# Optimization experiments

Hardware: AMD Instinct MI355X
Metric: run time of the kernel (lower is better)

## Reference

```python
import jax, jax.numpy as jnp
import numpy as np
import math

EMBED_DIM = 512
NUM_HEADS = 8
HEAD_DIM = EMBED_DIM // NUM_HEADS


def setup_inputs() -> dict:
    key = jax.random.key(0)
    ks = jax.random.split(key, 11)
    s = 1.0 / math.sqrt(EMBED_DIM)
    x = jax.random.normal(ks[0], (8, EMBED_DIM, 32, 32), dtype=jnp.float32)
    Wq = jax.random.uniform(ks[1], (EMBED_DIM, EMBED_DIM), jnp.float32, -s, s)
    bq = jax.random.uniform(ks[2], (EMBED_DIM,), jnp.float32, -s, s)
    Wk = jax.random.uniform(ks[3], (EMBED_DIM, EMBED_DIM), jnp.float32, -s, s)
    bk = jax.random.uniform(ks[4], (EMBED_DIM,), jnp.float32, -s, s)
    Wv = jax.random.uniform(ks[5], (EMBED_DIM, EMBED_DIM), jnp.float32, -s, s)
    bv = jax.random.uniform(ks[6], (EMBED_DIM,), jnp.float32, -s, s)
    Wo = jax.random.uniform(ks[7], (EMBED_DIM, EMBED_DIM), jnp.float32, -s, s)
    bo = jax.random.uniform(ks[8], (EMBED_DIM,), jnp.float32, -s, s)
    gamma = jnp.ones((EMBED_DIM,), jnp.float32)
    beta = jnp.zeros((EMBED_DIM,), jnp.float32)
    return {"x": x, "Wq": Wq, "bq": bq, "Wk": Wk, "bk": bk, "Wv": Wv,
            "bv": bv, "Wo": Wo, "bo": bo, "gamma": gamma, "beta": beta}


def layer_norm(x, gamma, beta, eps=1e-5):
    mu = jnp.mean(x, axis=-1, keepdims=True)
    var = jnp.mean(jnp.square(x - mu), axis=-1, keepdims=True)
    return (x - mu) * jax.lax.rsqrt(var + eps) * gamma + beta


def reference(x, Wq, bq, Wk, bk, Wv, bv, Wo, bo, gamma, beta):
    B, C, H, W = x.shape
    S = H * W
    # [B, S, C]
    x_flat = x.reshape(B, C, S).transpose(0, 2, 1)
    residual = x_flat
    xn = layer_norm(x_flat, gamma, beta)
    # torch Linear: y = x @ W^T + b
    q = (xn @ Wq.T + bq).reshape(B, S, NUM_HEADS, HEAD_DIM)
    k = (xn @ Wk.T + bk).reshape(B, S, NUM_HEADS, HEAD_DIM)
    v = (xn @ Wv.T + bv).reshape(B, S, NUM_HEADS, HEAD_DIM)
    scale = 1.0 / math.sqrt(HEAD_DIM)
    scores = jnp.einsum('bqhd,bkhd->bhqk', q, k) * scale
    attn = jax.nn.softmax(scores, axis=-1)  # dropout is identity in eval
    out = jnp.einsum('bhqk,bkhd->bqhd', attn, v).reshape(B, S, C)
    out = out @ Wo.T + bo + residual
    return out.transpose(0, 2, 1).reshape(B, C, H, W)
```

## Files before the change

### kernel.cpp

```cpp
#include <hip/hip_runtime.h>
#include <hip/hip_bf16.h>

typedef __bf16 bf16_t;
typedef __bf16 bf16x8 __attribute__((ext_vector_type(8)));
typedef float floatx4 __attribute__((ext_vector_type(4)));

#define EMBED 512
#define S_LEN 1024
#define NH 8
#define HD 64
#define LDK 1056
#define LDV 1088

#define MFMA16(a, b, c) __builtin_amdgcn_mfma_f32_16x16x32_bf16(a, b, c, 0, 0, 0)

static __device__ __forceinline__ bf16_t f2bf(float f) {
    unsigned int x = __builtin_bit_cast(unsigned int, f);
    unsigned int lsb = (x >> 16) & 1u;
    x += 0x7fffu + lsb;
    unsigned short u = (unsigned short)(x >> 16);
    return __builtin_bit_cast(bf16_t, u);
}
static __device__ __forceinline__ float bf2f(bf16_t v) {
    unsigned short u = __builtin_bit_cast(unsigned short, v);
    unsigned int x = ((unsigned int)u) << 16;
    return __builtin_bit_cast(float, x);
}
static __device__ __forceinline__ unsigned int pack2(float lo, float hi) {
    return (__builtin_bit_cast(unsigned int, lo) >> 16) |
           (__builtin_bit_cast(unsigned int, hi) & 0xFFFF0000u);
}
static __device__ __forceinline__ unsigned int pack2r(float lo, float hi) {
    unsigned short a = __builtin_bit_cast(unsigned short, f2bf(lo));
    unsigned short b = __builtin_bit_cast(unsigned short, f2bf(hi));
    return (unsigned int)a | ((unsigned int)b << 16);
}
static __device__ __forceinline__ void gload16(const bf16_t* g, bf16_t* l) {
    __builtin_amdgcn_global_load_lds(
        (const __attribute__((address_space(1))) unsigned int*)g,
        (__attribute__((address_space(3))) unsigned int*)l, 16, 0, 0);
}

__global__ __launch_bounds__(256) void ln_cvt_kernel(const float* __restrict__ x,
                                                     const float* __restrict__ gamma,
                                                     const float* __restrict__ beta,
                                                     bf16_t* __restrict__ xn,
                                                     const float* __restrict__ w0,
                                                     const float* __restrict__ w1,
                                                     const float* __restrict__ w2,
                                                     const float* __restrict__ w3,
                                                     bf16_t* __restrict__ d0,
                                                     bf16_t* __restrict__ d1,
                                                     bf16_t* __restrict__ d2,
                                                     bf16_t* __restrict__ d3) {
    __shared__ float T[16][521];
    __shared__ float Pm[16][65], Pq[16][65];
    __shared__ float Mu[16], Rs[16];
    int bid = blockIdx.x;
    int t = threadIdx.x;
    if (bid >= 512) {
        int cb2 = bid - 512;
        const float* s; bf16_t* d;
        switch (cb2 >> 7) {
            case 0:  s = w0; d = d0; break;
            case 1:  s = w1; d = d1; break;
            case 2:  s = w2; d = d2; break;
            default: s = w3; d = d3; break;
        }
        int i = ((cb2 & 127) * 256 + t) * 8;
#pragma unroll
        for (int j = 0; j < 8; ++j) d[i + j] = f2bf(s[i + j]);
        return;
    }
    int b = bid >> 6, s0 = (bid & 63) * 16;
    int lc = t >> 2;
    int si = (t & 3) * 4;
    const float* xp = x + ((size_t)b * EMBED + lc) * S_LEN + s0 + si;
    float sm[4] = {}, sq[4] = {};
#pragma unroll
    for (int p = 0; p < 8; ++p) {
        int c = lc + p * 64;
        float4 v = *(const float4*)(xp + (size_t)p * 64 * S_LEN);
        int cs = c ^ ((c >> 3) & 0x38);
        T[si + 0][cs] = v.x; T[si + 1][cs] = v.y;
        T[si + 2][cs] = v.z; T[si + 3][cs] = v.w;
        sm[0] += v.x; sq[0] += v.x * v.x;
        sm[1] += v.y; sq[1] += v.y * v.y;
        sm[2] += v.z; sq[2] += v.z * v.z;
        sm[3] += v.w; sq[3] += v.w * v.w;
    }
#pragma unroll
    for (int k = 0; k < 4; ++k) { Pm[si + k][lc] = sm[k]; Pq[si + k][lc] = sq[k]; }
    __syncthreads();
    if (t < 16) {
        float m = 0.f, q = 0.f;
#pragma unroll
        for (int j = 0; j < 64; ++j) { m += Pm[t][j]; q += Pq[t][j]; }
        float mu = m * (1.0f / EMBED);
        float var = q * (1.0f / EMBED) - mu * mu;
        Mu[t] = mu; Rs[t] = rsqrtf(var + 1e-5f);
    }
    __syncthreads();
    int cidx = t & 31;
    int rw = t >> 5;
#pragma unroll
    for (int rg = 0; rg < 2; ++rg) {
        int srl = rg * 8 + rw;
        float mu = Mu[srl], rs = Rs[srl];
        int cb = cidx * 16;
        bf16_t* dst = xn + ((size_t)b * S_LEN + s0 + srl) * EMBED + cb;
#pragma unroll
        for (int h = 0; h < 2; ++h) {
            int c0h = cb + h * 8;
            float4 g0 = *(const float4*)(gamma + c0h);
            float4 g1 = *(const float4*)(gamma + c0h + 4);
            float4 be0 = *(const float4*)(beta + c0h);
            float4 be1 = *(const float4*)(beta + c0h + 4);
            float gv[8] = {g0.x, g0.y, g0.z, g0.w, g1.x, g1.y, g1.z, g1.w};
            float bv[8] = {be0.x, be0.y, be0.z, be0.w, be1.x, be1.y, be1.z, be1.w};
            bf16x8 o;
#pragma unroll
            for (int j = 0; j < 8; ++j) {
                int c = c0h + j;
                int cs = c ^ ((c >> 3) & 0x38);
                o[j] = f2bf((T[srl][cs] - mu) * rs * gv[j] + bv[j]);
            }
            *(bf16x8*)(dst + h * 8) = o;
        }
    }
}

__global__ __launch_bounds__(256) void gemm_kernel(const bf16_t* __restrict__ X,
                                                   const bf16_t* __restrict__ W,
                                                   const float* __restrict__ b0,
                                                   const float* __restrict__ b1,
                                                   const float* __restrict__ b2,
                                                   bf16_t* __restrict__ Y,
                                                   bf16_t* __restrict__ vtb) {
    __shared__ __align__(16) bf16_t Sh[2][128 * 72];
    bf16_t* Wlin = &Sh[0][0];
    int t = threadIdx.x;
    int col0 = blockIdx.y * 128, row0 = blockIdx.x * 128;
    int lane = t & 63, w = t >> 6, g = lane >> 4, n16 = lane & 15;
    int swzk = (((lane & 7) ^ (lane >> 3)) & 7) * 8;
    const bf16_t* wg = W + (size_t)(col0 + w * 32 + (lane >> 3)) * EMBED + swzk;
    bf16_t* ldwave = Wlin + (w * 4) * 512;
    {
#pragma unroll
        for (int j = 0; j < 4; ++j)
            gload16(wg + (size_t)j * 8 * EMBED, ldwave + j * 512);
    }
    int rw0 = row0 + w * 32;
    const bf16_t* xr0 = X + (size_t)(rw0 + n16) * EMBED + g * 8;
    const bf16_t* xr1 = xr0 + (size_t)16 * EMBED;
    bf16x8 a00 = *(const bf16x8*)(xr0);
    bf16x8 a01 = *(const bf16x8*)(xr0 + 32);
    bf16x8 a10 = *(const bf16x8*)(xr1);
    bf16x8 a11 = *(const bf16x8*)(xr1 + 32);
    __syncthreads();
    floatx4 acc[2][8] = {};
    int cs0 = ((g ^ (n16 & 7))) * 8;
#pragma unroll
    for (int kc = 0; kc < 8; ++kc) {
        bf16x8 na00, na01, na10, na11;
        if (kc < 7) {
            int ko = (kc + 1) * 64;
            bf16_t* ld = Wlin + ((kc + 1) & 1) * 8192 + (w * 4) * 512;
#pragma unroll
            for (int j = 0; j < 4; ++j)
                gload16(wg + (size_t)j * 8 * EMBED + ko, ld + j * 512);
            na00 = *(const bf16x8*)(xr0 + ko);
            na01 = *(const bf16x8*)(xr0 + ko + 32);
            na10 = *(const bf16x8*)(xr1 + ko);
            na11 = *(const bf16x8*)(xr1 + ko + 32);
        }
        const bf16_t* wb = Wlin + (kc & 1) * 8192;
#pragma unroll
        for (int kk = 0; kk < 2; ++kk) {
            bf16x8 s0 = (kk == 0) ? a00 : a01;
            bf16x8 s1 = (kk == 0) ? a10 : a11;
            int csk = cs0 ^ (kk * 32);
#pragma unroll
            for (int nt = 0; nt < 8; ++nt) {
                bf16x8 bfr = *(const bf16x8*)(&wb[(nt * 16 + n16) * 64 + csk]);
                acc[0][nt] = MFMA16(s0, bfr, acc[0][nt]);
                acc[1][nt] = MFMA16(s1, bfr, acc[1][nt]);
            }
        }
        if (kc < 7) {
            a00 = na00; a01 = na01; a10 = na10; a11 = na11;
        }
        __syncthreads();
    }
    if (col0 < 1024) {
        const float* bp = (col0 < 512) ? b0 : b1;
#pragma unroll
        for (int ar = 0; ar < 2; ++ar)
#pragma unroll
            for (int nt = 0; nt < 8; ++nt) {
                int col = col0 + nt * 16 + n16;
                float bv = bp[col & 511];
#pragma unroll
                for (int r = 0; r < 4; ++r) {
                    int row = rw0 + ar * 16 + g * 4 + r;
                    Y[(size_t)row * LDK + col] = f2bf(acc[ar][nt][r] + bv);
                }
            }
    } else {
        bf16_t* Tl = Wlin;
#pragma unroll
        for (int ar = 0; ar < 2; ++ar)
#pragma unroll
            for (int nt = 0; nt < 8; ++nt) {
                int chl = nt * 16 + n16;
                float bv = b2[(col0 & 511) + chl];
                uint2 pr;
                pr.x = pack2r(acc[ar][nt][0] + bv, acc[ar][nt][1] + bv);
                pr.y = pack2r(acc[ar][nt][2] + bv, acc[ar][nt][3] + bv);
                *(uint2*)(&Tl[chl * 136 + w * 32 + ar * 16 + g * 4]) = pr;
            }
        __syncthreads();
        int ch = t >> 1, seg = (t & 1) * 64;
        int bb = row0 >> 10, s0 = row0 & 1023;
        bf16_t* dst = vtb + ((size_t)(bb * EMBED + (col0 - 1024) + ch)) * LDV + s0 + seg;
        const bf16_t* srcl = &Tl[ch * 136 + seg];
#pragma unroll
        for (int i = 0; i < 8; ++i)
            *(bf16x8*)(dst + i * 8) = *(const bf16x8*)(srcl + i * 8);
    }
}

__global__ __launch_bounds__(256) void wsgemm_out_kernel(const bf16_t* __restrict__ Wb,
                                                         const bf16_t* __restrict__ act,
                                                         const float* __restrict__ bias,
                                                         const float* __restrict__ xres,
                                                         float* __restrict__ out) {
    __shared__ __align__(16) bf16_t Al[2][64 * 72];
    int b = blockIdx.z, n0 = blockIdx.x * 64, m0 = blockIdx.y * 128;
    int t = threadIdx.x;
    int srow = t >> 2, sseg = (t & 3) * 16;
    const bf16_t* asrc = act + ((size_t)b * S_LEN + n0 + srow) * EMBED + sseg;
    {
        bf16x8 r0 = *(const bf16x8*)(asrc);
        bf16x8 r1 = *(const bf16x8*)(asrc + 8);
        bf16_t* d = &Al[0][srow * 72 + sseg];
        *(bf16x8*)d = r0; *(bf16x8*)(d + 8) = r1;
    }
    int lane = t & 63, w = t >> 6, g = lane >> 4, n16 = lane & 15;
    int mw = m0 + w * 32;
    const bf16_t* wr0 = Wb + (size_t)(mw + n16) * EMBED + g * 8;
    const bf16_t* wr1 = wr0 + (size_t)16 * EMBED;
    bf16x8 a00 = *(const bf16x8*)(wr0);
    bf16x8 a01 = *(const bf16x8*)(wr0 + 32);
    bf16x8 a10 = *(const bf16x8*)(wr1);
    bf16x8 a11 = *(const bf16x8*)(wr1 + 32);
    __syncthreads();
    floatx4 acc[2][4] = {};
#pragma unroll
    for (int kc = 0; kc < 8; ++kc) {
        bf16x8 p0, p1, na00, na01, na10, na11;
        if (kc < 7) {
            int ko = (kc + 1) * 64;
            p0 = *(const bf16x8*)(asrc + ko);
            p1 = *(const bf16x8*)(asrc + ko + 8);
            na00 = *(const bf16x8*)(wr0 + ko);
            na01 = *(const bf16x8*)(wr0 + ko + 32);
            na10 = *(const bf16x8*)(wr1 + ko);
            na11 = *(const bf16x8*)(wr1 + ko + 32);
        }
        const bf16_t* al = &Al[kc & 1][0];
#pragma unroll
        for (int kk = 0; kk < 2; ++kk) {
            bf16x8 s0 = (kk == 0) ? a00 : a01;
            bf16x8 s1 = (kk == 0) ? a10 : a11;
#pragma unroll
            for (int nt = 0; nt < 4; ++nt) {
                bf16x8 bfr = *(const bf16x8*)(&al[(nt * 16 + n16) * 72 + kk * 32 + g * 8]);
                acc[0][nt] = MFMA16(s0, bfr, acc[0][nt]);
                acc[1][nt] = MFMA16(s1, bfr, acc[1][nt]);
            }
        }
        if (kc < 7) {
            bf16_t* d = &Al[(kc + 1) & 1][srow * 72 + sseg];
            *(bf16x8*)d = p0; *(bf16x8*)(d + 8) = p1;
            a00 = na00; a01 = na01; a10 = na10; a11 = na11;
        }
        __syncthreads();
    }
#pragma unroll
    for (int ar = 0; ar < 2; ++ar)
#pragma unroll
        for (int r = 0; r < 4; ++r) {
            int row = mw + ar * 16 + g * 4 + r;
            float bv = bias[row];
#pragma unroll
            for (int nt = 0; nt < 4; ++nt) {
                int col = n0 + nt * 16 + n16;
                size_t oi = ((size_t)b * EMBED + row) * S_LEN + col;
                out[oi] = acc[ar][nt][r] + bv + xres[oi];
            }
        }
}

__global__ __launch_bounds__(256) void attn_kernel(const bf16_t* __restrict__ qk,
                                                   const bf16_t* __restrict__ vt,
                                                   bf16_t* __restrict__ o) {
    __shared__ __align__(16) bf16_t Kt[2][64 * 72];
    __shared__ __align__(16) bf16_t Vl2[2][64 * 72];
    __shared__ __align__(16) unsigned int Pl[4][16 * 68];
    int bid = blockIdx.x;
    int bh = bid & 63, qt = bid >> 6;
    int b = bh >> 3, h = bh & 7;
    int t = threadIdx.x, w = t >> 6, lane = t & 63, g = lane >> 4, n16 = lane & 15;
    size_t baseQK = (size_t)b * S_LEN * LDK;
    size_t baseV  = ((size_t)b * EMBED + h * HD) * LDV;
    int qA = qt * 128 + w * 32 + n16;

    const float QSC = 0.18033688f;
    const bf16_t* qpA = qk + baseQK + (size_t)qA * LDK + h * HD + g * 8;
    const bf16_t* qpB = qpA + (size_t)16 * LDK;
    bf16x8 qa0 = *(const bf16x8*)(qpA);
    bf16x8 qa1 = *(const bf16x8*)(qpA + 32);
    bf16x8 qb0 = *(const bf16x8*)(qpB);
    bf16x8 qb1 = *(const bf16x8*)(qpB + 32);
#pragma unroll
    for (int j = 0; j < 8; ++j) {
        qa0[j] = f2bf(bf2f(qa0[j]) * QSC);
        qa1[j] = f2bf(bf2f(qa1[j]) * QSC);
        qb0[j] = f2bf(bf2f(qb0[j]) * QSC);
        qb1[j] = f2bf(bf2f(qb1[j]) * QSC);
    }
    const bf16_t* kbase = qk + baseQK + 512 + h * HD;
    const bf16_t* vbase = vt + baseV;

    int srow = t >> 2, scol = (t & 3) * 16;
    const bf16_t* ksrc = kbase + (size_t)srow * LDK + scol;
    const bf16_t* vsrc = vbase + (size_t)srow * LDV + scol;
    {
        bf16x8 k0 = *(const bf16x8*)(ksrc);
        bf16x8 k1 = *(const bf16x8*)(ksrc + 8);
        bf16x8 v0 = *(const bf16x8*)(vsrc);
        bf16x8 v1 = *(const bf16x8*)(vsrc + 8);
        bf16_t* kd = &Kt[0][srow * 72 + scol];
        bf16_t* vd = &Vl2[0][srow * 72 + scol];
        *(bf16x8*)kd = k0; *(bf16x8*)(kd + 8) = k1;
        *(bf16x8*)vd = v0; *(bf16x8*)(vd + 8) = v1;
    }

    float lsA[4] = {}, lsB[4] = {};
    floatx4 oaccA[4] = {}, oaccB[4] = {};
    unsigned int* PLw = &Pl[w][0];
    const float NEG12L2E = -17.3123405f;

    for (int it = 0; it < 16; ++it) {
        int cur = it & 1, nxt = cur ^ 1;
        __syncthreads();
        bf16x8 pk0, pk1, pv0, pv1;
        if (it < 15) {
            const bf16_t* kp = ksrc + (size_t)(it + 1) * 64 * LDK;
            pk0 = *(const bf16x8*)(kp);
            pk1 = *(const bf16x8*)(kp + 8);
            const bf16_t* vp = vsrc + (it + 1) * 64;
            pv0 = *(const bf16x8*)(vp);
            pv1 = *(const bf16x8*)(vp + 8);
        }
        const bf16_t* Kl = &Kt[cur][0];
        const bf16_t* Vl = &Vl2[cur][0];
        floatx4 sA[4], sB[4];
#pragma unroll
        for (int kb = 0; kb < 4; ++kb) {
            bf16x8 k0 = *(const bf16x8*)(&Kl[(kb * 16 + n16) * 72 + g * 8]);
            bf16x8 k1 = *(const bf16x8*)(&Kl[(kb * 16 + n16) * 72 + 32 + g * 8]);
            sA[kb] = floatx4{NEG12L2E, NEG12L2E, NEG12L2E, NEG12L2E};
            sA[kb] = MFMA16(k0, qa0, sA[kb]);
            sA[kb] = MFMA16(k1, qa1, sA[kb]);
            sB[kb] = floatx4{NEG12L2E, NEG12L2E, NEG12L2E, NEG12L2E};
            sB[kb] = MFMA16(k0, qb0, sB[kb]);
            sB[kb] = MFMA16(k1, qb1, sB[kb]);
        }
#pragma unroll
        for (int kb = 0; kb < 4; ++kb)
#pragma unroll
            for (int r = 0; r < 4; ++r) {
                float eA = exp2f(sA[kb][r]);
                sA[kb][r] = eA; lsA[kb] += eA;
                float eB = exp2f(sB[kb][r]);
                sB[kb][r] = eB; lsB[kb] += eB;
            }
#pragma unroll
        for (int kb = 0; kb < 4; ++kb) {
            uint2 prA, prB;
            prA.x = pack2(sA[kb][0], sA[kb][1]);
            prA.y = pack2(sA[kb][2], sA[kb][3]);
            *(uint2*)&PLw[n16 * 68 + kb * 8 + g * 2] = prA;
            prB.x = pack2(sB[kb][0], sB[kb][1]);
            prB.y = pack2(sB[kb][2], sB[kb][3]);
            *(uint2*)&PLw[n16 * 68 + 32 + kb * 8 + g * 2] = prB;
        }
        uint4 uA0 = *(const uint4*)&PLw[n16 * 68 + g * 4];
        uint4 uA1 = *(const uint4*)&PLw[n16 * 68 + 16 + g * 4];
        uint4 uB0 = *(const uint4*)&PLw[n16 * 68 + 32 + g * 4];
        uint4 uB1 = *(const uint4*)&PLw[n16 * 68 + 48 + g * 4];
        bf16x8 pfA0 = __builtin_bit_cast(bf16x8, uA0);
        bf16x8 pfA1 = __builtin_bit_cast(bf16x8, uA1);
        bf16x8 pfB0 = __builtin_bit_cast(bf16x8, uB0);
        bf16x8 pfB1 = __builtin_bit_cast(bf16x8, uB1);
        if (it < 15) {
            bf16_t* kd = &Kt[nxt][srow * 72 + scol];
            bf16_t* vd = &Vl2[nxt][srow * 72 + scol];
            *(bf16x8*)kd = pk0; *(bf16x8*)(kd + 8) = pk1;
            *(bf16x8*)vd = pv0; *(bf16x8*)(vd + 8) = pv1;
        }
#pragma unroll
        for (int dt = 0; dt < 4; ++dt) {
            bf16x8 v0 = *(const bf16x8*)(&Vl[(dt * 16 + n16) * 72 + g * 8]);
            bf16x8 v1 = *(const bf16x8*)(&Vl[(dt * 16 + n16) * 72 + 32 + g * 8]);
            oaccA[dt] = MFMA16(v0, pfA0, oaccA[dt]);
            oaccA[dt] = MFMA16(v1, pfA1, oaccA[dt]);
            oaccB[dt] = MFMA16(v0, pfB0, oaccB[dt]);
            oaccB[dt] = MFMA16(v1, pfB1, oaccB[dt]);
        }
    }
    float lA = (lsA[0] + lsA[1]) + (lsA[2] + lsA[3]);
    lA += __shfl_xor(lA, 16);
    lA += __shfl_xor(lA, 32);
    float lB = (lsB[0] + lsB[1]) + (lsB[2] + lsB[3]);
    lB += __shfl_xor(lB, 16);
    lB += __shfl_xor(lB, 32);
    float rlA = 1.0f / lA, rlB = 1.0f / lB;
    size_t orowA = ((size_t)b * S_LEN + qA) * EMBED + h * HD;
    size_t orowB = orowA + (size_t)16 * EMBED;
#pragma unroll
    for (int dt = 0; dt < 4; ++dt) {
        uint2 prA, prB;
        prA.x = pack2(oaccA[dt][0] * rlA, oaccA[dt][1] * rlA);
        prA.y = pack2(oaccA[dt][2] * rlA, oaccA[dt][3] * rlA);
        *(uint2*)(o + orowA + dt * 16 + g * 4) = prA;
        prB.x = pack2(oaccB[dt][0] * rlB, oaccB[dt][1] * rlB);
        prB.y = pack2(oaccB[dt][2] * rlB, oaccB[dt][3] * rlB);
        *(uint2*)(o + orowB + dt * 16 + g * 4) = prB;
    }
}

extern "C" void kernel_launch(void* const* d_in, const int* in_sizes, int n_in,
                              void* d_out, int out_size, void* d_ws, size_t ws_size,
                              hipStream_t stream) {
    const float* x     = (const float*)d_in[0];
    const float* Wq    = (const float*)d_in[1];
    const float* bq    = (const float*)d_in[2];
    const float* Wk    = (const float*)d_in[3];
    const float* bk    = (const float*)d_in[4];
    const float* Wv    = (const float*)d_in[5];
    const float* bv    = (const float*)d_in[6];
    const float* Wo    = (const float*)d_in[7];
    const float* bo    = (const float*)d_in[8];
    const float* gamma = (const float*)d_in[9];
    const float* beta  = (const float*)d_in[10];
    float* out = (float*)d_out;

    char* ws = (char*)d_ws;
    bf16_t* xn    = (bf16_t*)ws;
    bf16_t* qkb   = (bf16_t*)(ws + 8388608);
    bf16_t* wqkv  = (bf16_t*)(ws + 25690112);
    bf16_t* wo    = (bf16_t*)(ws + 27262976);
    bf16_t* ab    = xn;

    bf16_t* vtb = (bf16_t*)d_out;

    ln_cvt_kernel<<<dim3(1024), 256, 0, stream>>>(x, gamma, beta, xn,
                                                  Wq, Wk, Wv, Wo,
                                                  wqkv, wqkv + 262144,
                                                  wqkv + 524288, wo);
    gemm_kernel<<<dim3(64, 12), 256, 0, stream>>>(xn, wqkv, bq, bk, bv, qkb, vtb);
    attn_kernel<<<dim3(512), 256, 0, stream>>>(qkb, vtb, ab);
    wsgemm_out_kernel<<<dim3(16, 4, 8), 256, 0, stream>>>(wo, ab, bo, x, out);
}
```

Baseline: 170.0 us.

## Deepen K/V prefetch to two tiles ahead with unrolled even/odd iterations

New measurement: 169.0 us. About the same (-0.6%).

```diff
diff --git a/kernel.cpp b/kernel.cpp
--- a/kernel.cpp
+++ b/kernel.cpp
@@ -346,81 +346,121 @@
         *(bf16x8*)kd = k0; *(bf16x8*)(kd + 8) = k1;
         *(bf16x8*)vd = v0; *(bf16x8*)(vd + 8) = v1;
     }
+    bf16x8 rkO0, rkO1, rvO0, rvO1, rkE0, rkE1, rvE0, rvE1;
+    {
+        const bf16_t* kp = ksrc + (size_t)64 * LDK;
+        rkO0 = *(const bf16x8*)(kp);
+        rkO1 = *(const bf16x8*)(kp + 8);
+        const bf16_t* vp = vsrc + 64;
+        rvO0 = *(const bf16x8*)(vp);
+        rvO1 = *(const bf16x8*)(vp + 8);
+    }
 
     float lsA[4] = {}, lsB[4] = {};
     floatx4 oaccA[4] = {}, oaccB[4] = {};
     unsigned int* PLw = &Pl[w][0];
     const float NEG12L2E = -17.3123405f;
-
-    for (int it = 0; it < 16; ++it) {
-        int cur = it & 1, nxt = cur ^ 1;
+    bf16x8 pfA0, pfA1, pfB0, pfB1;
+
+#define ATTN_QKSM(CUR)                                                        \
+    {                                                                         \
+        const bf16_t* Kl = &Kt[CUR][0];                                       \
+        floatx4 sA[4], sB[4];                                                 \
+        _Pragma("unroll")                                                     \
+        for (int kb = 0; kb < 4; ++kb) {                                      \
+            bf16x8 k0 = *(const bf16x8*)(&Kl[(kb * 16 + n16) * 72 + g * 8]);  \
+            bf16x8 k1 = *(const bf16x8*)(&Kl[(kb * 16 + n16) * 72 + 32 + g * 8]); \
+            sA[kb] = floatx4{NEG12L2E, NEG12L2E, NEG12L2E, NEG12L2E};         \
+            sA[kb] = MFMA16(k0, qa0, sA[kb]);                                 \
+            sA[kb] = MFMA16(k1, qa1, sA[kb]);                                 \
+            sB[kb] = floatx4{NEG12L2E, NEG12L2E, NEG12L2E, NEG12L2E};         \
+            sB[kb] = MFMA16(k0, qb0, sB[kb]);                                 \
+            sB[kb] = MFMA16(k1, qb1, sB[kb]);                                 \
+        }                                                                     \
+        _Pragma("unroll")                                                     \
+        for (int kb = 0; kb < 4; ++kb)                                        \
+            _Pragma("unroll")                                                 \
+            for (int r = 0; r < 4; ++r) {                                     \
+                float eA = exp2f(sA[kb][r]);                                  \
+                sA[kb][r] = eA; lsA[kb] += eA;                                \
+                float eB = exp2f(sB[kb][r]);                                  \
+                sB[kb][r] = eB; lsB[kb] += eB;                                \
+            }                                                                 \
+        _Pragma("unroll")                                                     \
+        for (int kb = 0; kb < 4; ++kb) {                                      \
+            uint2 prA, prB;                                                   \
+            prA.x = pack2(sA[kb][0], sA[kb][1]);                              \
+            prA.y = pack2(sA[kb][2], sA[kb][3]);                              \
+            *(uint2*)&PLw[n16 * 68 + kb * 8 + g * 2] = prA;                   \
+            prB.x = pack2(sB[kb][0], sB[kb][1]);                              \
+            prB.y = pack2(sB[kb][2], sB[kb][3]);                              \
+            *(uint2*)&PLw[n16 * 68 + 32 + kb * 8 + g * 2] = prB;              \
+        }                                                                     \
+        uint4 uA0 = *(const uint4*)&PLw[n16 * 68 + g * 4];                    \
+        uint4 uA1 = *(const uint4*)&PLw[n16 * 68 + 16 + g * 4];               \
+        uint4 uB0 = *(const uint4*)&PLw[n16 * 68 + 32 + g * 4];               \
+        uint4 uB1 = *(const uint4*)&PLw[n16 * 68 + 48 + g * 4];               \
+        pfA0 = __builtin_bit_cast(bf16x8, uA0);                               \
+        pfA1 = __builtin_bit_cast(bf16x8, uA1);                               \
+        pfB0 = __builtin_bit_cast(bf16x8, uB0);                               \
+        pfB1 = __builtin_bit_cast(bf16x8, uB1);                               \
+    }
+
+#define ATTN_PV(CUR)                                                          \
+    {                                                                         \
+        const bf16_t* Vl = &Vl2[CUR][0];                                      \
+        _Pragma("unroll")                                                     \
+        for (int dt = 0; dt < 4; ++dt) {                                      \
+            bf16x8 v0 = *(const bf16x8*)(&Vl[(dt * 16 + n16) * 72 + g * 8]);  \
+            bf16x8 v1 = *(const bf16x8*)(&Vl[(dt * 16 + n16) * 72 + 32 + g * 8]); \
+            oaccA[dt] = MFMA16(v0, pfA0, oaccA[dt]);                          \
+            oaccA[dt] = MFMA16(v1, pfA1, oaccA[dt]);                          \
+            oaccB[dt] = MFMA16(v0, pfB0, oaccB[dt]);                          \
+            oaccB[dt] = MFMA16(v1, pfB1, oaccB[dt]);                          \
+        }                                                                     \
+    }
+
+    for (int ih = 0; ih < 8; ++ih) {
+        int itE = ih * 2;
+        int itO = itE + 1;
         __syncthreads();
-        bf16x8 pk0, pk1, pv0, pv1;
-        if (it < 15) {
-            const bf16_t* kp = ksrc + (size_t)(it + 1) * 64 * LDK;
-            pk0 = *(const bf16x8*)(kp);
-            pk1 = *(const bf16x8*)(kp + 8);
-            const bf16_t* vp = vsrc + (it + 1) * 64;
-            pv0 = *(const bf16x8*)(vp);
-            pv1 = *(const bf16x8*)(vp + 8);
-        }
-        const bf16_t* Kl = &Kt[cur][0];
-        const bf16_t* Vl = &Vl2[cur][0];
-        floatx4 sA[4], sB[4];
-#pragma unroll
-        for (int kb = 0; kb < 4; ++kb) {
-            bf16x8 k0 = *(const bf16x8*)(&Kl[(kb * 16 + n16) * 72 + g * 8]);
-            bf16x8 k1 = *(const bf16x8*)(&Kl[(kb * 16 + n16) * 72 + 32 + g * 8]);
-            sA[kb] = floatx4{NEG12L2E, NEG12L2E, NEG12L2E, NEG12L2E};
-            sA[kb] = MFMA16(k0, qa0, sA[kb]);
-            sA[kb] = MFMA16(k1, qa1, sA[kb]);
-            sB[kb] = floatx4{NEG12L2E, NEG12L2E, NEG12L2E, NEG12L2E};
-            sB[kb] = MFMA16(k0, qb0, sB[kb]);
-            sB[kb] = MFMA16(k1, qb1, sB[kb]);
-        }
-#pragma unroll
-        for (int kb = 0; kb < 4; ++kb)
-#pragma unroll
-            for (int r = 0; r < 4; ++r) {
-                float eA = exp2f(sA[kb][r]);
-                sA[kb][r] = eA; lsA[kb] += eA;
-                float eB = exp2f(sB[kb][r]);
-                sB[kb][r] = eB; lsB[kb] += eB;
-            }
-#pragma unroll
-        for (int kb = 0; kb < 4; ++kb) {
-            uint2 prA, prB;
-            prA.x = pack2(sA[kb][0], sA[kb][1]);
-            prA.y = pack2(sA[kb][2], sA[kb][3]);
-            *(uint2*)&PLw[n16 * 68 + kb * 8 + g * 2] = prA;
-            prB.x = pack2(sB[kb][0], sB[kb][1]);
-            prB.y = pack2(sB[kb][2], sB[kb][3]);
-            *(uint2*)&PLw[n16 * 68 + 32 + kb * 8 + g * 2] = prB;
-        }
-        uint4 uA0 = *(const uint4*)&PLw[n16 * 68 + g * 4];
-        uint4 uA1 = *(const uint4*)&PLw[n16 * 68 + 16 + g * 4];
-        uint4 uB0 = *(const uint4*)&PLw[n16 * 68 + 32 + g * 4];
-        uint4 uB1 = *(const uint4*)&PLw[n16 * 68 + 48 + g * 4];
-        bf16x8 pfA0 = __builtin_bit_cast(bf16x8, uA0);
-        bf16x8 pfA1 = __builtin_bit_cast(bf16x8, uA1);
-        bf16x8 pfB0 = __builtin_bit_cast(bf16x8, uB0);
-        bf16x8 pfB1 = __builtin_bit_cast(bf16x8, uB1);
-        if (it < 15) {
-            bf16_t* kd = &Kt[nxt][srow * 72 + scol];
-            bf16_t* vd = &Vl2[nxt][srow * 72 + scol];
-            *(bf16x8*)kd = pk0; *(bf16x8*)(kd + 8) = pk1;
-            *(bf16x8*)vd = pv0; *(bf16x8*)(vd + 8) = pv1;
-        }
-#pragma unroll
-        for (int dt = 0; dt < 4; ++dt) {
-            bf16x8 v0 = *(const bf16x8*)(&Vl[(dt * 16 + n16) * 72 + g * 8]);
-            bf16x8 v1 = *(const bf16x8*)(&Vl[(dt * 16 + n16) * 72 + 32 + g * 8]);
-            oaccA[dt] = MFMA16(v0, pfA0, oaccA[dt]);
-            oaccA[dt] = MFMA16(v1, pfA1, oaccA[dt]);
-            oaccB[dt] = MFMA16(v0, pfB0, oaccB[dt]);
-            oaccB[dt] = MFMA16(v1, pfB1, oaccB[dt]);
-        }
-    }
+        if (itE < 14) {
+            const bf16_t* kp = ksrc + (size_t)(itE + 2) * 64 * LDK;
+            rkE0 = *(const bf16x8*)(kp);
+            rkE1 = *(const bf16x8*)(kp + 8);
+            const bf16_t* vp = vsrc + (itE + 2) * 64;
+            rvE0 = *(const bf16x8*)(vp);
+            rvE1 = *(const bf16x8*)(vp + 8);
+        }
+        ATTN_QKSM(0)
+        {
+            bf16_t* kd = &Kt[1][srow * 72 + scol];
+            bf16_t* vd = &Vl2[1][srow * 72 + scol];
+            *(bf16x8*)kd = rkO0; *(bf16x8*)(kd + 8) = rkO1;
+            *(bf16x8*)vd = rvO0; *(bf16x8*)(vd + 8) = rvO1;
+        }
+        ATTN_PV(0)
+        __syncthreads();
+        if (itO < 14) {
+            const bf16_t* kp = ksrc + (size_t)(itO + 2) * 64 * LDK;
+            rkO0 = *(const bf16x8*)(kp);
+            rkO1 = *(const bf16x8*)(kp + 8);
+            const bf16_t* vp = vsrc + (itO + 2) * 64;
+            rvO0 = *(const bf16x8*)(vp);
+            rvO1 = *(const bf16x8*)(vp + 8);
+        }
+        ATTN_QKSM(1)
+        if (itO < 15) {
+            bf16_t* kd = &Kt[0][srow * 72 + scol];
+            bf16_t* vd = &Vl2[0][srow * 72 + scol];
+            *(bf16x8*)kd = rkE0; *(bf16x8*)(kd + 8) = rkE1;
+            *(bf16x8*)vd = rvE0; *(bf16x8*)(vd + 8) = rvE1;
+        }
+        ATTN_PV(1)
+    }
+#undef ATTN_QKSM
+#undef ATTN_PV
+
     float lA = (lsA[0] + lsA[1]) + (lsA[2] + lsA[3]);
     lA += __shfl_xor(lA, 16);
     lA += __shfl_xor(lA, 32);
```
